# Optimization experiments

Hardware: AMD Instinct MI355X
Metric: run time of the kernel (lower is better)

Reference implementation:

```python
import jax, jax.numpy as jnp
import numpy as np

N_NODES = 50000
N_EDGES = 600000
H_DIM = 128


def setup_inputs() -> dict:
    key = jax.random.key(0)
    ks = jax.random.split(key, 16)
    s = 0.05  # weight scale
    inp = {
        'h': jax.random.normal(ks[0], (N_NODES, H_DIM), jnp.float32),
        'coord': jax.random.normal(ks[1], (N_NODES, 3), jnp.float32),
        'edge_index': jax.random.randint(ks[2], (2, N_EDGES), 0, N_NODES, jnp.int32),
        # edge_mlp: (2*input_nf + 1) -> hidden -> hidden
        'w_e1': jax.random.normal(ks[3], (2 * H_DIM + 1, H_DIM), jnp.float32) * s,
        'b_e1': jnp.zeros((H_DIM,), jnp.float32),
        'w_e2': jax.random.normal(ks[4], (H_DIM, H_DIM), jnp.float32) * s,
        'b_e2': jnp.zeros((H_DIM,), jnp.float32),
        # node_mlp: (hidden + input_nf) -> hidden -> output_nf
        'w_n1': jax.random.normal(ks[5], (2 * H_DIM, H_DIM), jnp.float32) * s,
        'b_n1': jnp.zeros((H_DIM,), jnp.float32),
        'w_n2': jax.random.normal(ks[6], (H_DIM, H_DIM), jnp.float32) * s,
        'b_n2': jnp.zeros((H_DIM,), jnp.float32),
        # coord_mlp: hidden -> hidden -> 1 (last layer xavier gain 0.001, no bias)
        'w_c1': jax.random.normal(ks[7], (H_DIM, H_DIM), jnp.float32) * s,
        'b_c1': jnp.zeros((H_DIM,), jnp.float32),
        'w_c2': jax.random.normal(ks[8], (H_DIM, 1), jnp.float32) * 0.001,
    }
    return inp


def reference(h, coord, edge_index, w_e1, b_e1, w_e2, b_e2,
              w_n1, b_n1, w_n2, b_n2, w_c1, b_c1, w_c2):
    silu = jax.nn.silu
    n = h.shape[0]
    row, col = edge_index[0], edge_index[1]

    # coord2radial (normalize=False)
    coord_diff = coord[row] - coord[col]                 # [E, 3]
    radial = jnp.sum(coord_diff ** 2, axis=1, keepdims=True)  # [E, 1]

    # edge model (no attention, no edge_attr)
    edge_in = jnp.concatenate([h[row], h[col], radial], axis=1)  # [E, 257]
    edge_feat = silu(silu(edge_in @ w_e1 + b_e1) @ w_e2 + b_e2)  # [E, H]

    # coord model: coords_agg='mean', tanh=False
    w = silu(edge_feat @ w_c1 + b_c1) @ w_c2             # [E, 1]
    trans = coord_diff * w                               # [E, 3]
    t_sum = jax.ops.segment_sum(trans, row, num_segments=n)
    cnt = jax.ops.segment_sum(jnp.ones((row.shape[0], 1), trans.dtype), row,
                              num_segments=n)
    coord_new = coord + t_sum / jnp.maximum(cnt, 1.0)

    # node model (residual=True, no graphnorm, no node attention)
    agg = jax.ops.segment_sum(edge_feat, row, num_segments=n)   # [N, H]
    node_in = jnp.concatenate([h, agg], axis=1)                 # [N, 2H]
    h_new = h + (silu(node_in @ w_n1 + b_n1) @ w_n2 + b_n2)

    return (h_new, coord_new, edge_feat)
```

## Files before the change

kernel.cpp:

```cpp
#include <hip/hip_runtime.h>

#define NN 50000
#define NE 600000

typedef __attribute__((ext_vector_type(8))) short short8;
typedef __attribute__((ext_vector_type(4))) float f32x4;

#define SWZ(row) ((((row) & 7) << 4) ^ (((row) & 8) << 2))

__device__ __forceinline__ float silu_f(float x) { return x / (1.0f + __expf(-x)); }

__device__ __forceinline__ unsigned short f2bf(float f) {
    unsigned u = __builtin_bit_cast(unsigned, f);
    unsigned r = u + 0x7FFFu + ((u >> 16) & 1u);
    return (unsigned short)(r >> 16);
}

__device__ __forceinline__ void lds_barrier() {
    asm volatile("s_waitcnt lgkmcnt(0)" ::: "memory");
    __builtin_amdgcn_s_barrier();
    asm volatile("" ::: "memory");
}

__device__ __forceinline__ void xpose4(float v[4]) {
    const int p = threadIdx.x & 3;
    float s0 = (p & 1) ? v[0] : v[1];
    float s1 = (p & 1) ? v[2] : v[3];
    s0 = __shfl_xor(s0, 1);
    s1 = __shfl_xor(s1, 1);
    float w0 = (p & 1) ? s0 : v[0];
    float w1 = (p & 1) ? v[1] : s0;
    float w2 = (p & 1) ? s1 : v[2];
    float w3 = (p & 1) ? v[3] : s1;
    float t0 = (p & 2) ? w0 : w2;
    float t1 = (p & 2) ? w1 : w3;
    t0 = __shfl_xor(t0, 2);
    t1 = __shfl_xor(t1, 2);
    v[0] = (p & 2) ? t0 : w0;
    v[2] = (p & 2) ? w2 : t0;
    v[1] = (p & 2) ? t1 : w1;
    v[3] = (p & 2) ? w3 : t1;
}

__device__ __forceinline__ unsigned cvt_pk_bf16(float lo, float hi) {
    unsigned r;
    asm("v_cvt_pk_bf16_f32 %0, %1, %2" : "=v"(r) : "v"(lo), "v"(hi));
    return r;
}

__global__ __launch_bounds__(512) void k_prep(const float* __restrict__ h,
                                              unsigned short* __restrict__ hb)
{
    const int nchunks = NN * 128 / 8;
    for (int i = blockIdx.x * blockDim.x + threadIdx.x; i < nchunks;
         i += gridDim.x * blockDim.x) {
        const float4* p = (const float4*)(h + (size_t)i * 8);
        float4 x = p[0], y = p[1];
        short8 v;
        v[0] = f2bf(x.x); v[1] = f2bf(x.y); v[2] = f2bf(x.z); v[3] = f2bf(x.w);
        v[4] = f2bf(y.x); v[5] = f2bf(y.y); v[6] = f2bf(y.z); v[7] = f2bf(y.w);
        *(short8*)(hb + (size_t)i * 8) = v;
    }
}

__global__ __launch_bounds__(256) void k_deg(const int* __restrict__ ei,
                                             int* __restrict__ deg)
{
    for (int e = blockIdx.x * 256 + threadIdx.x; e < NE; e += gridDim.x * 256)
        atomicAdd(&deg[ei[e]], 1);
}

__global__ __launch_bounds__(1024) void k_scan(const int* __restrict__ deg,
                                               int* __restrict__ rowptr,
                                               int* __restrict__ cursor)
{
    __shared__ int sb[1024];
    const int t = threadIdx.x;
    const int CH = 49;
    const int base = t * CH;
    int s = 0;
    for (int j = 0; j < CH; ++j) {
        int idx = base + j;
        if (idx < NN) s += deg[idx];
    }
    sb[t] = s;
    __syncthreads();
    for (int off = 1; off < 1024; off <<= 1) {
        int v = (t >= off) ? sb[t - off] : 0;
        __syncthreads();
        sb[t] += v;
        __syncthreads();
    }
    int run = sb[t] - s;
    for (int j = 0; j < CH; ++j) {
        int idx = base + j;
        if (idx < NN) {
            rowptr[idx] = run;
            cursor[idx] = run;
            run += deg[idx];
        }
    }
    if (t == 1023) rowptr[NN] = sb[1023];
}

__global__ __launch_bounds__(256) void k_scatter(const int* __restrict__ ei,
                                                 int* __restrict__ cursor,
                                                 int* __restrict__ elist)
{
    for (int e = blockIdx.x * 256 + threadIdx.x; e < NE; e += gridDim.x * 256) {
        int pos = atomicAdd(&cursor[ei[e]], 1);
        elist[pos] = e;
    }
}

__global__ __launch_bounds__(512, 8) void k_edge(
    const unsigned short* __restrict__ hb, const float* __restrict__ coord,
    const int* __restrict__ ei, const int* __restrict__ elist,
    const float* __restrict__ w_e1, const float* __restrict__ b_e1,
    const float* __restrict__ w_e2, const float* __restrict__ b_e2,
    float* __restrict__ ef, float* __restrict__ agg)
{
    __shared__ unsigned short A1s[64 * 256];
    __shared__ unsigned short A2s[64 * 128];
    __shared__ float rad[64];
    __shared__ int   es_s[64];
    __shared__ int   seg_start[65];
    __shared__ int   seg_row[64];
    __shared__ int   nseg_s;

    const int tid  = threadIdx.x;
    const int wv   = tid >> 6, lane = tid & 63;
    const int l4   = lane >> 4, li = lane & 15;
    const int n    = wv * 16 + li;

    short8 bw1[8], bw2[4];
    #pragma unroll
    for (int ks = 0; ks < 8; ++ks) {
        short8 t;
        #pragma unroll
        for (int j = 0; j < 8; ++j) t[j] = f2bf(w_e1[(ks * 32 + l4 * 8 + j) * 128 + n]);
        bw1[ks] = t;
    }
    #pragma unroll
    for (int ks = 0; ks < 4; ++ks) {
        short8 t;
        #pragma unroll
        for (int j = 0; j < 8; ++j) t[j] = f2bf(w_e2[(ks * 32 + l4 * 8 + j) * 128 + n]);
        bw2[ks] = t;
    }
    const float wradv = w_e1[256 * 128 + n];
    const float b1v = b_e1[n], b2v = b_e2[n];

    const f32x4 z4 = {0.f, 0.f, 0.f, 0.f};
    const int colb = wv * 16 + (li >> 2) * 4;
    const int pp   = li & 3;

    for (int t = blockIdx.x; t < NE / 64; t += gridDim.x) {
        const int ebase = t * 64;
        if (tid < 64) {
            int e = elist[ebase + tid];
            int r = ei[e], c = ei[NE + e];
            es_s[tid] = e;
            float dx = coord[r * 3 + 0] - coord[c * 3 + 0];
            float dy = coord[r * 3 + 1] - coord[c * 3 + 1];
            float dz = coord[r * 3 + 2] - coord[c * 3 + 2];
            rad[tid] = dx * dx + dy * dy + dz * dz;
            int prev = __shfl_up(r, 1);
            bool flag = (lane == 0) || (r != prev);
            unsigned long long mask = __ballot(flag);
            if (flag) {
                int pos = __popcll(mask & ((1ull << lane) - 1ull));
                seg_start[pos] = lane;
                seg_row[pos]   = r;
            }
            if (lane == 0) {
                int ns = __popcll(mask);
                nseg_s = ns;
                seg_start[ns] = 64;
            }
        }
        {
            int le = tid >> 3;
            int e = elist[ebase + le];
            int r = ei[e], c = ei[NE + e];
            const unsigned short* hr = hb + (size_t)r * 128;
            const unsigned short* hc = hb + (size_t)c * 128;
            #pragma unroll
            for (int i = 0; i < 4; ++i) {
                int chunk = i * 8 + (tid & 7);
                short8 v = (chunk < 16) ? *(const short8*)(hr + chunk * 8)
                                        : *(const short8*)(hc + (chunk - 16) * 8);
                int off = le * 512 + ((chunk * 16) ^ SWZ(le));
                *(short8*)((char*)A1s + off) = v;
            }
        }
        lds_barrier();

        f32x4 acc[4];
        acc[0] = z4; acc[1] = z4; acc[2] = z4; acc[3] = z4;
        for (int ks = 0; ks < 8; ++ks) {
            const int kb = ks * 64 + l4 * 16;
            #pragma unroll
            for (int mf = 0; mf < 4; ++mf) {
                int row = mf * 16 + li;
                short8 a = *(const short8*)((const char*)A1s + row * 512 + (kb ^ SWZ(row)));
                acc[mf] = __builtin_amdgcn_mfma_f32_16x16x32_bf16(a, bw1[ks], acc[mf], 0, 0, 0);
            }
        }
        #pragma unroll
        for (int mf = 0; mf < 4; ++mf) {
            float4 rr = *(const float4*)&rad[mf * 16 + l4 * 4];
            float v[4];
            v[0] = silu_f(acc[mf][0] + rr.x * wradv + b1v);
            v[1] = silu_f(acc[mf][1] + rr.y * wradv + b1v);
            v[2] = silu_f(acc[mf][2] + rr.z * wradv + b1v);
            v[3] = silu_f(acc[mf][3] + rr.w * wradv + b1v);
            xpose4(v);
            int row = mf * 16 + l4 * 4 + pp;
            uint2 d;
            d.x = cvt_pk_bf16(v[0], v[1]);
            d.y = cvt_pk_bf16(v[2], v[3]);
            *(uint2*)((char*)A2s + row * 256 + ((colb * 2) ^ SWZ(row))) = d;
        }
        lds_barrier();

        acc[0] = z4; acc[1] = z4; acc[2] = z4; acc[3] = z4;
        for (int ks = 0; ks < 4; ++ks) {
            const int kb = ks * 64 + l4 * 16;
            #pragma unroll
            for (int mf = 0; mf < 4; ++mf) {
                int row = mf * 16 + li;
                short8 a = *(const short8*)((const char*)A2s + row * 256 + (kb ^ SWZ(row)));
                acc[mf] = __builtin_amdgcn_mfma_f32_16x16x32_bf16(a, bw2[ks], acc[mf], 0, 0, 0);
            }
        }
        #pragma unroll
        for (int mf = 0; mf < 4; ++mf) {
            float v[4];
            v[0] = silu_f(acc[mf][0] + b2v);
            v[1] = silu_f(acc[mf][1] + b2v);
            v[2] = silu_f(acc[mf][2] + b2v);
            v[3] = silu_f(acc[mf][3] + b2v);
            xpose4(v);
            int row = mf * 16 + l4 * 4 + pp;
            uint2 d;
            d.x = cvt_pk_bf16(v[0], v[1]);
            d.y = cvt_pk_bf16(v[2], v[3]);
            *(uint2*)((char*)A1s + row * 256 + ((colb * 2) ^ SWZ(row))) = d;
            int e = es_s[row];
            f32x4 o = {v[0], v[1], v[2], v[3]};
            __builtin_nontemporal_store(o, (f32x4*)&ef[(size_t)e * 128 + colb]);
        }
        lds_barrier();

        {
            const int cg = tid & 31;
            const int ns = nseg_s;
            for (int s = tid >> 5; s < ns; s += 16) {
                int i0 = seg_start[s], i1 = seg_start[s + 1];
                float s0 = 0.f, s1 = 0.f, s2 = 0.f, s3 = 0.f;
                for (int i = i0; i < i1; ++i) {
                    uint2 d = *(const uint2*)((const char*)A1s + i * 256 + ((cg * 8) ^ SWZ(i)));
                    s0 += __builtin_bit_cast(float, d.x << 16);
                    s1 += __builtin_bit_cast(float, d.x & 0xffff0000u);
                    s2 += __builtin_bit_cast(float, d.y << 16);
                    s3 += __builtin_bit_cast(float, d.y & 0xffff0000u);
                }
                float* ap = &agg[(size_t)seg_row[s] * 128 + cg * 4];
                atomicAdd(ap + 0, s0);
                atomicAdd(ap + 1, s1);
                atomicAdd(ap + 2, s2);
                atomicAdd(ap + 3, s3);
            }
        }
        lds_barrier();
    }
}

__global__ __launch_bounds__(512, 4) void k_coord(
    const float* __restrict__ ef, const float* __restrict__ coord,
    const int* __restrict__ ei,
    const float* __restrict__ w_c1, const float* __restrict__ b_c1,
    const float* __restrict__ w_c2,
    float* __restrict__ tsum)
{
    __shared__ unsigned short EFs[128 * 128];
    __shared__ float wqp[4][128];

    const int tid  = threadIdx.x;
    const int wv   = tid >> 6, lane = tid & 63;
    const int l4   = lane >> 4, li = lane & 15;
    const int eh   = (wv & 1) * 64;
    const int fq   = (wv >> 1) * 32;

    short8 wa[2][4];
    #pragma unroll
    for (int mf = 0; mf < 2; ++mf)
        #pragma unroll
        for (int ks = 0; ks < 4; ++ks) {
            short8 t;
            #pragma unroll
            for (int j = 0; j < 8; ++j)
                t[j] = f2bf(w_c1[(ks * 32 + l4 * 8 + j) * 128 + fq + mf * 16 + li]);
            wa[mf][ks] = t;
        }
    float bcv[2][4], wcv[2][4];
    #pragma unroll
    for (int mf = 0; mf < 2; ++mf)
        #pragma unroll
        for (int r = 0; r < 4; ++r) {
            int feat = fq + mf * 16 + l4 * 4 + r;
            bcv[mf][r] = b_c1[feat];
            wcv[mf][r] = w_c2[feat];
        }

    const f32x4 z4 = {0.f, 0.f, 0.f, 0.f};
    const int ntiles = (NE + 127) / 128;

    for (int t = blockIdx.x; t < ntiles; t += gridDim.x) {
        const int ebase = t * 128;
        {
            int row = tid >> 2;
            int e = ebase + row;
            int cb = (tid & 3) * 32;
            #pragma unroll
            for (int i = 0; i < 2; ++i) {
                int c0 = cb + i * 16;
                short8 v;
                if (e < NE) {
                    const float4* p = (const float4*)(ef + (size_t)e * 128 + c0);
                    float4 x = p[0], y = p[1];
                    v[0] = f2bf(x.x); v[1] = f2bf(x.y); v[2] = f2bf(x.z); v[3] = f2bf(x.w);
                    v[4] = f2bf(y.x); v[5] = f2bf(y.y); v[6] = f2bf(y.z); v[7] = f2bf(y.w);
                } else v = (short8)0;
                *(short8*)((char*)EFs + row * 256 + ((c0 * 2) ^ SWZ(row))) = v;
                int c1 = c0 + 8;
                short8 w;
                if (e < NE) {
                    const float4* q = (const float4*)(ef + (size_t)e * 128 + c1);
                    float4 x = q[0], y = q[1];
                    w[0] = f2bf(x.x); w[1] = f2bf(x.y); w[2] = f2bf(x.z); w[3] = f2bf(x.w);
                    w[4] = f2bf(y.x); w[5] = f2bf(y.y); w[6] = f2bf(y.z); w[7] = f2bf(y.w);
                } else w = (short8)0;
                *(short8*)((char*)EFs + row * 256 + ((c1 * 2) ^ SWZ(row))) = w;
            }
        }
        lds_barrier();

        f32x4 acc[2][4];
        #pragma unroll
        for (int mf = 0; mf < 2; ++mf)
            #pragma unroll
            for (int nf = 0; nf < 4; ++nf) acc[mf][nf] = z4;
        for (int ks = 0; ks < 4; ++ks) {
            const int kb = ks * 64 + l4 * 16;
            #pragma unroll
            for (int nf = 0; nf < 4; ++nf) {
                int edge = eh + nf * 16 + li;
                short8 b = *(const short8*)((const char*)EFs + edge * 256 + (kb ^ SWZ(edge)));
                #pragma unroll
                for (int mf = 0; mf < 2; ++mf)
                    acc[mf][nf] = __builtin_amdgcn_mfma_f32_16x16x32_bf16(
                        wa[mf][ks], b, acc[mf][nf], 0, 0, 0);
            }
        }
        #pragma unroll
        for (int nf = 0; nf < 4; ++nf) {
            float p = 0.f;
            #pragma unroll
            for (int mf = 0; mf < 2; ++mf)
                #pragma unroll
                for (int r = 0; r < 4; ++r)
                    p += silu_f(acc[mf][nf][r] + bcv[mf][r]) * wcv[mf][r];
            p += __shfl_xor(p, 16);
            p += __shfl_xor(p, 32);
            if (l4 == 0) wqp[wv >> 1][eh + nf * 16 + li] = p;
        }
        lds_barrier();

        if (tid < 128) {
            float wq = wqp[0][tid] + wqp[1][tid] + wqp[2][tid] + wqp[3][tid];
            int e = ebase + tid;
            if (e < NE) {
                int r = ei[e], c = ei[NE + e];
                float dx = coord[r * 3 + 0] - coord[c * 3 + 0];
                float dy = coord[r * 3 + 1] - coord[c * 3 + 1];
                float dz = coord[r * 3 + 2] - coord[c * 3 + 2];
                atomicAdd(&tsum[r * 3 + 0], dx * wq);
                atomicAdd(&tsum[r * 3 + 1], dy * wq);
                atomicAdd(&tsum[r * 3 + 2], dz * wq);
            }
        }
    }
}

__global__ __launch_bounds__(512, 8) void k_node(
    const unsigned short* __restrict__ hb, const float* __restrict__ h,
    const float* __restrict__ agg,
    const float* __restrict__ w_n1, const float* __restrict__ b_n1,
    const float* __restrict__ w_n2, const float* __restrict__ b_n2,
    const float* __restrict__ coord, const float* __restrict__ tsum,
    const int* __restrict__ rowptr,
    float* __restrict__ h_new, float* __restrict__ coord_new)
{
    __shared__ unsigned short As[64 * 256];
    __shared__ unsigned short Us[64 * 128];

    const int tid  = threadIdx.x;
    const int wv   = tid >> 6, lane = tid & 63;
    const int l4   = lane >> 4, li = lane & 15;
    const int n    = wv * 16 + li;

    short8 bw1[8], bw2[4];
    #pragma unroll
    for (int ks = 0; ks < 8; ++ks) {
        short8 t;
        #pragma unroll
        for (int j = 0; j < 8; ++j) t[j] = f2bf(w_n1[(ks * 32 + l4 * 8 + j) * 128 + n]);
        bw1[ks] = t;
    }
    #pragma unroll
    for (int ks = 0; ks < 4; ++ks) {
        short8 t;
        #pragma unroll
        for (int j = 0; j < 8; ++j) t[j] = f2bf(w_n2[(ks * 32 + l4 * 8 + j) * 128 + n]);
        bw2[ks] = t;
    }
    const float b1v = b_n1[n], b2v = b_n2[n];

    const f32x4 z4 = {0.f, 0.f, 0.f, 0.f};
    const int ntiles = (NN + 63) / 64;
    const int colb = wv * 16 + (li >> 2) * 4;
    const int pp   = li & 3;

    for (int t = blockIdx.x; t < ntiles; t += gridDim.x) {
        const int nbase = t * 64;
        {
            int ln = tid >> 3;
            int node = nbase + ln;
            #pragma unroll
            for (int i = 0; i < 4; ++i) {
                int chunk = i * 8 + (tid & 7);
                short8 v;
                if (node < NN) {
                    if (chunk < 16) {
                        v = *(const short8*)(hb + (size_t)node * 128 + chunk * 8);
                    } else {
                        const float4* p = (const float4*)(agg + (size_t)node * 128 + (chunk - 16) * 8);
                        float4 x = p[0], y = p[1];
                        v[0] = f2bf(x.x); v[1] = f2bf(x.y); v[2] = f2bf(x.z); v[3] = f2bf(x.w);
                        v[4] = f2bf(y.x); v[5] = f2bf(y.y); v[6] = f2bf(y.z); v[7] = f2bf(y.w);
                    }
                } else v = (short8)0;
                int off = ln * 512 + ((chunk * 16) ^ SWZ(ln));
                *(short8*)((char*)As + off) = v;
            }
        }
        lds_barrier();

        f32x4 acc[4];
        acc[0] = z4; acc[1] = z4; acc[2] = z4; acc[3] = z4;
        for (int ks = 0; ks < 8; ++ks) {
            const int kb = ks * 64 + l4 * 16;
            #pragma unroll
            for (int mf = 0; mf < 4; ++mf) {
                int row = mf * 16 + li;
                short8 a = *(const short8*)((const char*)As + row * 512 + (kb ^ SWZ(row)));
                acc[mf] = __builtin_amdgcn_mfma_f32_16x16x32_bf16(a, bw1[ks], acc[mf], 0, 0, 0);
            }
        }
        #pragma unroll
        for (int mf = 0; mf < 4; ++mf) {
            float v[4];
            v[0] = silu_f(acc[mf][0] + b1v);
            v[1] = silu_f(acc[mf][1] + b1v);
            v[2] = silu_f(acc[mf][2] + b1v);
            v[3] = silu_f(acc[mf][3] + b1v);
            xpose4(v);
            int row = mf * 16 + l4 * 4 + pp;
            uint2 d;
            d.x = cvt_pk_bf16(v[0], v[1]);
            d.y = cvt_pk_bf16(v[2], v[3]);
            *(uint2*)((char*)Us + row * 256 + ((colb * 2) ^ SWZ(row))) = d;
        }
        lds_barrier();

        acc[0] = z4; acc[1] = z4; acc[2] = z4; acc[3] = z4;
        for (int ks = 0; ks < 4; ++ks) {
            const int kb = ks * 64 + l4 * 16;
            #pragma unroll
            for (int mf = 0; mf < 4; ++mf) {
                int row = mf * 16 + li;
                short8 a = *(const short8*)((const char*)Us + row * 256 + (kb ^ SWZ(row)));
                acc[mf] = __builtin_amdgcn_mfma_f32_16x16x32_bf16(a, bw2[ks], acc[mf], 0, 0, 0);
            }
        }
        #pragma unroll
        for (int mf = 0; mf < 4; ++mf) {
            float v[4];
            v[0] = acc[mf][0] + b2v;
            v[1] = acc[mf][1] + b2v;
            v[2] = acc[mf][2] + b2v;
            v[3] = acc[mf][3] + b2v;
            xpose4(v);
            int row = mf * 16 + l4 * 4 + pp;
            int node = nbase + row;
            if (node < NN) {
                const f32x4 h4 = *(const f32x4*)&h[(size_t)node * 128 + colb];
                f32x4 o = {v[0] + h4.x, v[1] + h4.y, v[2] + h4.z, v[3] + h4.w};
                __builtin_nontemporal_store(o, (f32x4*)&h_new[(size_t)node * 128 + colb]);
            }
        }
        if (tid < 64) {
            int node = nbase + tid;
            if (node < NN) {
                int deg = rowptr[node + 1] - rowptr[node];
                float m = fmaxf((float)deg, 1.0f);
                coord_new[node * 3 + 0] = coord[node * 3 + 0] + tsum[node * 3 + 0] / m;
                coord_new[node * 3 + 1] = coord[node * 3 + 1] + tsum[node * 3 + 1] / m;
                coord_new[node * 3 + 2] = coord[node * 3 + 2] + tsum[node * 3 + 2] / m;
            }
        }
    }
}

extern "C" void kernel_launch(void* const* d_in, const int* in_sizes, int n_in,
                              void* d_out, int out_size, void* d_ws, size_t ws_size,
                              hipStream_t stream)
{
    const float* h     = (const float*)d_in[0];
    const float* coord = (const float*)d_in[1];
    const int*   ei    = (const int*)d_in[2];
    const float* w_e1  = (const float*)d_in[3];
    const float* b_e1  = (const float*)d_in[4];
    const float* w_e2  = (const float*)d_in[5];
    const float* b_e2  = (const float*)d_in[6];
    const float* w_n1  = (const float*)d_in[7];
    const float* b_n1  = (const float*)d_in[8];
    const float* w_n2  = (const float*)d_in[9];
    const float* b_n2  = (const float*)d_in[10];
    const float* w_c1  = (const float*)d_in[11];
    const float* b_c1  = (const float*)d_in[12];
    const float* w_c2  = (const float*)d_in[13];

    float* h_new     = (float*)d_out;
    float* coord_new = h_new + (size_t)NN * 128;
    float* ef        = coord_new + (size_t)NN * 3;

    float*          agg    = (float*)d_ws;
    float*          tsum   = agg + (size_t)NN * 128;
    int*            deg    = (int*)(tsum + (size_t)NN * 3);
    int*            rowptr = deg + NN;
    int*            cursor = rowptr + NN + 1;
    int*            elist  = cursor + NN;
    unsigned short* hb     = (unsigned short*)(elist + NE);

    hipMemsetAsync(agg, 0, ((size_t)NN * 128 + (size_t)NN * 3 + NN) * sizeof(float), stream);

    k_prep   <<<1024, 512, 0, stream>>>(h, hb);
    k_deg    <<<1024, 256, 0, stream>>>(ei, deg);
    k_scan   <<<1,   1024, 0, stream>>>(deg, rowptr, cursor);
    k_scatter<<<1024, 256, 0, stream>>>(ei, cursor, elist);
    k_edge   <<<768,  512, 0, stream>>>(hb, coord, ei, elist, w_e1, b_e1,
                                        w_e2, b_e2, ef, agg);
    k_coord  <<<512,  512, 0, stream>>>(ef, coord, ei, w_c1, b_c1, w_c2, tsum);
    k_node   <<<768,  512, 0, stream>>>(hb, h, agg, w_n1, b_n1, w_n2, b_n2,
                                        coord, tsum, rowptr, h_new, coord_new);
}
```

Before: 632.6 us.

## Prefetch next tile's gathered node features in edge kernel via registers

The edge kernel now loads the next tile's bf16 h[row]/h[col] rows into registers while the current tile's MFMAs run, then writes them to LDS at the start of the next iteration. This hides the gather latency behind compute. The extra registers force a lower launch-bounds occupancy hint (8 to 6 waves per EU). The coord kernel grid is also enlarged from 512 to 1536 blocks.

New measurement: 787.1 us. 1.24x slower.

```diff
diff --git a/kernel.cpp b/kernel.cpp
--- a/kernel.cpp
+++ b/kernel.cpp
@@ -113,7 +113,7 @@
     }
 }
 
-__global__ __launch_bounds__(512, 8) void k_edge(
+__global__ __launch_bounds__(512, 6) void k_edge(
     const unsigned short* __restrict__ hb, const float* __restrict__ coord,
     const int* __restrict__ ei, const int* __restrict__ elist,
     const float* __restrict__ w_e1, const float* __restrict__ b_e1,
@@ -154,8 +154,26 @@
     const f32x4 z4 = {0.f, 0.f, 0.f, 0.f};
     const int colb = wv * 16 + (li >> 2) * 4;
     const int pp   = li & 3;
-
-    for (int t = blockIdx.x; t < NE / 64; t += gridDim.x) {
+    const int le   = tid >> 3;
+    const int ch0  = tid & 7;
+    const int ntiles = NE / 64;
+    const int tstep  = gridDim.x;
+
+    short8 pf[4];
+    {
+        int e = elist[blockIdx.x * 64 + le];
+        int r = ei[e], c = ei[NE + e];
+        const unsigned short* hr = hb + (size_t)r * 128;
+        const unsigned short* hc = hb + (size_t)c * 128;
+        #pragma unroll
+        for (int i = 0; i < 4; ++i) {
+            int chunk = i * 8 + ch0;
+            pf[i] = (chunk < 16) ? *(const short8*)(hr + chunk * 8)
+                                 : *(const short8*)(hc + (chunk - 16) * 8);
+        }
+    }
+
+    for (int t = blockIdx.x; t < ntiles; t += tstep) {
         const int ebase = t * 64;
         if (tid < 64) {
             int e = elist[ebase + tid];
@@ -179,22 +197,29 @@
                 seg_start[ns] = 64;
             }
         }
+        #pragma unroll
+        for (int i = 0; i < 4; ++i) {
+            int chunk = i * 8 + ch0;
+            int off = le * 512 + ((chunk * 16) ^ SWZ(le));
+            *(short8*)((char*)A1s + off) = pf[i];
+        }
+        lds_barrier();
+
         {
-            int le = tid >> 3;
-            int e = elist[ebase + le];
-            int r = ei[e], c = ei[NE + e];
-            const unsigned short* hr = hb + (size_t)r * 128;
-            const unsigned short* hc = hb + (size_t)c * 128;
-            #pragma unroll
-            for (int i = 0; i < 4; ++i) {
-                int chunk = i * 8 + (tid & 7);
-                short8 v = (chunk < 16) ? *(const short8*)(hr + chunk * 8)
-                                        : *(const short8*)(hc + (chunk - 16) * 8);
-                int off = le * 512 + ((chunk * 16) ^ SWZ(le));
-                *(short8*)((char*)A1s + off) = v;
-            }
-        }
-        lds_barrier();
+            int tn = t + tstep;
+            if (tn < ntiles) {
+                int e = elist[tn * 64 + le];
+                int r = ei[e], c = ei[NE + e];
+                const unsigned short* hr = hb + (size_t)r * 128;
+                const unsigned short* hc = hb + (size_t)c * 128;
+                #pragma unroll
+                for (int i = 0; i < 4; ++i) {
+                    int chunk = i * 8 + ch0;
+                    pf[i] = (chunk < 16) ? *(const short8*)(hr + chunk * 8)
+                                         : *(const short8*)(hc + (chunk - 16) * 8);
+                }
+            }
+        }
 
         f32x4 acc[4];
         acc[0] = z4; acc[1] = z4; acc[2] = z4; acc[3] = z4;
@@ -563,7 +588,7 @@
     k_scatter<<<1024, 256, 0, stream>>>(ei, cursor, elist);
     k_edge   <<<768,  512, 0, stream>>>(hb, coord, ei, elist, w_e1, b_e1,
                                         w_e2, b_e2, ef, agg);
-    k_coord  <<<512,  512, 0, stream>>>(ef, coord, ei, w_c1, b_c1, w_c2, tsum);
+    k_coord  <<<1536, 512, 0, stream>>>(ef, coord, ei, w_c1, b_c1, w_c2, tsum);
     k_node   <<<768,  512, 0, stream>>>(hb, h, agg, w_n1, b_n1, w_n2, b_n2,
                                         coord, tsum, rowptr, h_new, coord_new);
 }
```
